# Kernel tuning notes

Hardware: AMD Instinct MI355X
Metric: run time of the kernel (lower is better)

Reference implementation:

```python
import jax, jax.numpy as jnp
import numpy as np

B, LQ, LK, C = 16, 1024, 1024, 512
WH = int(LQ ** 0.5)  # 32


def setup_inputs() -> dict:
    key = jax.random.key(0)
    ks = jax.random.split(key, 6)
    s1 = 1.0 / np.sqrt(LK)
    return {
        "query": jax.random.normal(ks[0], (B, LQ, C), jnp.float32),
        "key": jax.random.normal(ks[1], (B, LK, C), jnp.float32),
        "value": jax.random.normal(ks[2], (B, LK, C), jnp.float32),
        # nn.Linear weights, stored [out_features, in_features] like torch
        "w1": jax.random.normal(ks[3], (LK, LK), jnp.float32) * s1,
        "w2": jax.random.normal(ks[4], (LK, LK), jnp.float32) * s1,
        "w3": jax.random.normal(ks[5], (1, LK), jnp.float32) * s1,
    }


def reference(query, key, value, w1, w2, w3):
    # cosine-similarity matrix (computed under no_grad in the original)
    q = query / 100.0
    k = key / 100.0
    qn = jnp.sqrt(jnp.sum(q * q, axis=-1))[:, :, None]   # [B, LQ, 1]
    kn = jnp.sqrt(jnp.sum(k * k, axis=-1))[:, None, :]   # [B, 1, LK]
    outer = qn * kn                                       # rank-1 outer product [B, LQ, LK]
    upper = jnp.einsum('bqc,bkc->bqk', q, k)              # [B, LQ, LK]
    similar_rev = jax.lax.stop_gradient(upper / (outer + 1e-6))

    # 3-layer MLP gating over the LK axis -> scalar weight per query row
    h = jax.nn.gelu(jnp.einsum('bqk,ok->bqo', similar_rev, w1), approximate=False)
    h = jax.nn.gelu(jnp.einsum('bqk,ok->bqo', h, w2), approximate=False)
    w = jnp.einsum('bqk,ok->bqo', h, w3)[..., 0]          # [B, LQ]

    # weight^T @ similar_rev / wh, then tanh -> per-key scalar gate [B, LK, 1]
    weight = jnp.einsum('bq,bqk->bk', w, similar_rev) / WH
    weight = jnp.tanh(weight)[:, :, None]

    # value modulation + residual
    return value * weight + value
```

## Files before the change

kernel.cpp:

```cpp
#include <hip/hip_runtime.h>
#include <hip/hip_bf16.h>

#define B_  16
#define LQ_ 1024
#define LK_ 1024
#define C_  512

typedef __attribute__((ext_vector_type(4))) float f32x4;
typedef __attribute__((ext_vector_type(8))) short bf16x8;

__device__ __forceinline__ float bf2f(ushort u) {
  union { unsigned int i; float f; } v; v.i = ((unsigned int)u) << 16; return v.f;
}
__device__ __forceinline__ ushort f2bf(float f) {
  union { float f; unsigned int i; } v; v.f = f;
  unsigned int r = v.i + 0x7fffu + ((v.i >> 16) & 1u);
  return (ushort)(r >> 16);
}
__device__ __forceinline__ float gelu_fast(float x) {
  float u = x * (0.7978845608f + 0.0356774081f * x * x);
  u = fminf(fmaxf(u, -9.f), 9.f);
  float e = __expf(2.f * u);
  float t = (e - 1.f) / (e + 1.f);
  return 0.5f * x * (1.f + t);
}

__device__ __forceinline__ void gload_lds16(const ushort* g, ushort* l) {
  __builtin_amdgcn_global_load_lds(
      (const __attribute__((address_space(1))) void*)g,
      (__attribute__((address_space(3))) void*)l, 16, 0, 0);
}

__global__ __launch_bounds__(256) void prep_qk(const float* __restrict__ x,
                                               ushort* __restrict__ xb,
                                               float* __restrict__ norms) {
  int wid = blockIdx.x * 4 + (threadIdx.x >> 6);
  int lane = threadIdx.x & 63;
  const float* xr = x + (long)wid * C_;
  ushort* xo = xb + (long)wid * C_;
  float ss = 0.f;
#pragma unroll
  for (int i0 = 0; i0 < 2; ++i0) {
    int i = lane * 4 + i0 * 256;
    float4 v = *(const float4*)(xr + i);
    ss += v.x * v.x + v.y * v.y + v.z * v.z + v.w * v.w;
    ushort4 o;
    o.x = f2bf(v.x); o.y = f2bf(v.y); o.z = f2bf(v.z); o.w = f2bf(v.w);
    *(ushort4*)(xo + i) = o;
  }
#pragma unroll
  for (int off = 32; off > 0; off >>= 1) ss += __shfl_xor(ss, off);
  if (lane == 0) norms[wid] = sqrtf(ss);
}

__global__ __launch_bounds__(256) void conv_bf16(const float* __restrict__ x,
                                                 ushort* __restrict__ o, int n4) {
  int i = blockIdx.x * 256 + threadIdx.x;
  if (i < n4) {
    float4 v = *(const float4*)(x + (long)i * 4);
    ushort4 u;
    u.x = f2bf(v.x); u.y = f2bf(v.y); u.z = f2bf(v.z); u.w = f2bf(v.w);
    *(ushort4*)(o + (long)i * 4) = u;
  }
}

#define BK 32

template <int EPI>
__device__ __forceinline__ void tile128(
    const ushort* __restrict__ A, const ushort* __restrict__ Bm,
    ushort* __restrict__ Cc, int K, int bm, int bn, int b,
    const float* __restrict__ qn, const float* __restrict__ kn,
    const float* __restrict__ w3v, float* __restrict__ wv,
    ushort* smem) {
  int tid = threadIdx.x;
  int lane = tid & 63, w = tid >> 6;
  int wr = w >> 1, wc = w & 1;
  int l16 = lane & 15, lhi = lane >> 4;

  f32x4 acc[4][4] = {};

  int c0 = tid, c1 = tid + 256;
  int r0 = c0 >> 2, cb0 = (c0 & 3) ^ ((r0 >> 1) & 3);
  int r1 = c1 >> 2, cb1 = (c1 & 3) ^ ((r1 >> 1) & 3);
  int wb0 = (tid & ~63) * 8;
  int wb1 = wb0 + 256 * 8;

  const ushort* Ar0 = A + (long)(bm + r0) * K + cb0 * 8;
  const ushort* Ar1 = A + (long)(bm + r1) * K + cb1 * 8;
  const ushort* Br0 = Bm + (long)(bn + r0) * K + cb0 * 8;
  const ushort* Br1 = Bm + (long)(bn + r1) * K + cb1 * 8;

  const int nt = K / BK;
  gload_lds16(Ar0, smem + wb0);
  gload_lds16(Ar1, smem + wb1);
  gload_lds16(Br0, smem + 8192 + wb0);
  gload_lds16(Br1, smem + 8192 + wb1);
  __syncthreads();

  int cur = 0;
  for (int t = 0; t < nt; ++t) {
    if (t + 1 < nt) {
      int k1 = (t + 1) * BK;
      int nx = (cur ^ 1) * 4096;
      gload_lds16(Ar0 + k1, smem + nx + wb0);
      gload_lds16(Ar1 + k1, smem + nx + wb1);
      gload_lds16(Br0 + k1, smem + 8192 + nx + wb0);
      gload_lds16(Br1 + k1, smem + 8192 + nx + wb1);
    }

    const ushort* Ac = smem + cur * 4096;
    const ushort* Bc = smem + 8192 + cur * 4096;
    bf16x8 af[4], bfr[4];
#pragma unroll
    for (int m = 0; m < 4; ++m) {
      int r = wr * 64 + m * 16 + l16;
      af[m] = *(const bf16x8*)(Ac + r * 32 + ((lhi ^ ((r >> 1) & 3)) * 8));
    }
#pragma unroll
    for (int n = 0; n < 4; ++n) {
      int r = wc * 64 + n * 16 + l16;
      bfr[n] = *(const bf16x8*)(Bc + r * 32 + ((lhi ^ ((r >> 1) & 3)) * 8));
    }
#pragma unroll
    for (int m = 0; m < 4; ++m)
#pragma unroll
      for (int n = 0; n < 4; ++n)
        acc[m][n] = __builtin_amdgcn_mfma_f32_16x16x32_bf16(af[m], bfr[n],
                                                            acc[m][n], 0, 0, 0);
    __syncthreads();
    cur ^= 1;
  }

  if constexpr (EPI == 2) {
    float* wvb = wv + (long)b * LQ_;
    float w3c[4];
#pragma unroll
    for (int n = 0; n < 4; ++n) w3c[n] = w3v[bn + wc * 64 + n * 16 + l16];
#pragma unroll
    for (int m = 0; m < 4; ++m)
#pragma unroll
      for (int rr = 0; rr < 4; ++rr) {
        float s = 0.f;
#pragma unroll
        for (int n = 0; n < 4; ++n)
          s += gelu_fast(acc[m][n][rr]) * w3c[n];
        s += __shfl_xor(s, 1);
        s += __shfl_xor(s, 2);
        s += __shfl_xor(s, 4);
        s += __shfl_xor(s, 8);
        if (l16 == 0)
          atomicAdd(&wvb[bm + wr * 64 + m * 16 + lhi * 4 + rr], s);
      }
  } else {
    const float* qnb = qn + (long)b * LQ_;
    const float* knb = kn + (long)b * LK_;
#pragma unroll
    for (int m = 0; m < 4; ++m) {
      int row0 = bm + wr * 64 + m * 16 + lhi * 4;
#pragma unroll
      for (int n = 0; n < 4; ++n) {
        int col = bn + wc * 64 + n * 16 + l16;
#pragma unroll
        for (int rr = 0; rr < 4; ++rr) {
          float v = acc[m][n][rr];
          int grow = row0 + rr;
          if (EPI == 0) {
            v = v / (qnb[grow] * knb[col] + 1e-2f);
          } else {
            v = gelu_fast(v);
          }
          Cc[(long)grow * 1024 + col] = f2bf(v);
        }
      }
    }
  }
}

template <int EPI>
__device__ __forceinline__ void gemm_pair_body(
    const ushort* __restrict__ A, const ushort* __restrict__ Bm,
    ushort* __restrict__ Cc, int K, long sA, long sB, long sC,
    const float* __restrict__ qn, const float* __restrict__ kn,
    const float* __restrict__ w3v, float* __restrict__ wv) {
  int per = (int)(gridDim.x >> 3);
  int orig = blockIdx.x;
  int id = (orig & 7) * per + (orig >> 3);
  int b = id >> 5;
  int rp = id & 31;
  const int bm = (rp >> 2) * 128, bn0 = (rp & 3) * 256;

  A += (long)b * sA;
  Bm += (long)b * sB;
  if (EPI != 2) Cc += (long)b * sC;

  __shared__ ushort smem[16384];
  tile128<EPI>(A, Bm, Cc, K, bm, bn0, b, qn, kn, w3v, wv, smem);
  tile128<EPI>(A, Bm, Cc, K, bm, bn0 + 128, b, qn, kn, w3v, wv, smem);
}

__global__ __launch_bounds__(256, 2) void gemm_s(
    const ushort* __restrict__ A, const ushort* __restrict__ Bm,
    ushort* __restrict__ Cc, const float* __restrict__ qn,
    const float* __restrict__ kn) {
  gemm_pair_body<0>(A, Bm, Cc, C_, (long)LQ_ * C_, (long)LK_ * C_,
                    (long)LQ_ * LK_, qn, kn, nullptr, nullptr);
}

__global__ __launch_bounds__(256, 2) void gemm_h1(
    const ushort* __restrict__ A, const ushort* __restrict__ Bm,
    ushort* __restrict__ Cc) {
  gemm_pair_body<1>(A, Bm, Cc, LK_, (long)LQ_ * LK_, 0L, (long)LQ_ * LK_,
                    nullptr, nullptr, nullptr, nullptr);
}

__global__ __launch_bounds__(256, 2) void gemm_h2w(
    const ushort* __restrict__ A, const ushort* __restrict__ Bm,
    const float* __restrict__ w3v, float* __restrict__ wv) {
  gemm_pair_body<2>(A, Bm, nullptr, LK_, (long)LQ_ * LK_, 0L, 0L,
                    nullptr, nullptr, w3v, wv);
}

__global__ __launch_bounds__(256) void gate_partial(const ushort* __restrict__ S,
                                                    const float* __restrict__ wv,
                                                    float* __restrict__ wraw) {
  int b = blockIdx.z;
  int k = blockIdx.x * 256 + threadIdx.x;
  int q0 = blockIdx.y * 128;
  const ushort* Sb = S + (long)b * LQ_ * LK_;
  const float* wb = wv + b * LQ_;
  float acc = 0.f;
#pragma unroll 4
  for (int q = q0; q < q0 + 128; ++q) acc += wb[q] * bf2f(Sb[(long)q * LK_ + k]);
  atomicAdd(&wraw[b * LK_ + k], acc);
}

__global__ __launch_bounds__(256) void finalize(const float* __restrict__ value,
                                                const float* __restrict__ wraw,
                                                float* __restrict__ out) {
  long i = (long)blockIdx.x * 256 + threadIdx.x;
  long e = i * 4;
  int row = (int)(e >> 9);
  float g = 1.f + tanhf(wraw[row] * (1.f / 32.f));
  float4 v = ((const float4*)value)[i];
  v.x *= g; v.y *= g; v.z *= g; v.w *= g;
  ((float4*)out)[i] = v;
}

extern "C" void kernel_launch(void* const* d_in, const int* in_sizes, int n_in,
                              void* d_out, int out_size, void* d_ws,
                              size_t ws_size, hipStream_t stream) {
  const float* query = (const float*)d_in[0];
  const float* key   = (const float*)d_in[1];
  const float* value = (const float*)d_in[2];
  const float* w1    = (const float*)d_in[3];
  const float* w2    = (const float*)d_in[4];
  const float* w3    = (const float*)d_in[5];
  float* out = (float*)d_out;

  const size_t QB_BYTES = (size_t)B_ * LQ_ * C_ * 2;
  const size_t S_BYTES  = (size_t)B_ * LQ_ * LK_ * 2;
  const size_t W_BYTES  = (size_t)LK_ * LK_ * 2;
  const size_t OFF_QB = 0;
  const size_t OFF_KB = OFF_QB + QB_BYTES;
  const size_t OFF_S  = OFF_KB + QB_BYTES;
  const size_t OFF_H1 = OFF_S + S_BYTES;
  const size_t OFF_W1 = OFF_H1 + S_BYTES;
  const size_t OFF_W2 = OFF_W1 + W_BYTES;
  const size_t OFF_QN = OFF_W2 + W_BYTES;
  const size_t OFF_KN = OFF_QN + (size_t)B_ * LQ_ * 4;
  const size_t OFF_WV = OFF_KN + (size_t)B_ * LK_ * 4;
  const size_t OFF_WR = OFF_WV + (size_t)B_ * LQ_ * 4;
  const size_t TOTAL  = OFF_WR + (size_t)B_ * LK_ * 4;
  if (ws_size < TOTAL) return;

  char* ws = (char*)d_ws;
  ushort* Qb  = (ushort*)(ws + OFF_QB);
  ushort* Kb  = (ushort*)(ws + OFF_KB);
  ushort* S   = (ushort*)(ws + OFF_S);
  ushort* h1  = (ushort*)(ws + OFF_H1);
  ushort* W1b = (ushort*)(ws + OFF_W1);
  ushort* W2b = (ushort*)(ws + OFF_W2);
  float* qn   = (float*)(ws + OFF_QN);
  float* kn   = (float*)(ws + OFF_KN);
  float* wv   = (float*)(ws + OFF_WV);
  float* wraw = (float*)(ws + OFF_WR);

  prep_qk<<<dim3(B_ * LQ_ / 4), 256, 0, stream>>>(query, Qb, qn);
  prep_qk<<<dim3(B_ * LK_ / 4), 256, 0, stream>>>(key, Kb, kn);
  conv_bf16<<<dim3(LK_ * LK_ / 4 / 256), 256, 0, stream>>>(w1, W1b, LK_ * LK_ / 4);
  conv_bf16<<<dim3(LK_ * LK_ / 4 / 256), 256, 0, stream>>>(w2, W2b, LK_ * LK_ / 4);
  hipMemsetAsync(wraw, 0, (size_t)B_ * LK_ * 4, stream);
  hipMemsetAsync(wv, 0, (size_t)B_ * LQ_ * 4, stream);

  gemm_s<<<dim3(512), 256, 0, stream>>>(Qb, Kb, S, qn, kn);

  gemm_h1<<<dim3(512), 256, 0, stream>>>(S, W1b, h1);

  gemm_h2w<<<dim3(512), 256, 0, stream>>>(h1, W2b, w3, wv);

  gate_partial<<<dim3(LK_ / 256, LQ_ / 128, B_), 256, 0, stream>>>(S, wv, wraw);

  finalize<<<dim3((size_t)B_ * LK_ * C_ / 4 / 256), 256, 0, stream>>>(value, wraw, out);
}
```

Measured before the change: 184.7 us.

## Fuse prep kernels, use one 128x128 tile per GEMM block, vectorize gate

Merges the four conversion/norm launches into one prep kernel that dispatches rows by warp index. Each GEMM block now computes a single 128x128 tile instead of two adjacent tiles, which doubles the grid to 1024 blocks for better CU occupancy and load balance. In exchange, the A-tile reuse across the paired N tiles is lost. The gate reduction now has each thread read four bf16 values with one vector load over 64 query rows, with fewer blocks and more atomics per thread.

```diff
diff --git a/kernel.cpp b/kernel.cpp
--- a/kernel.cpp
+++ b/kernel.cpp
@@ -31,48 +31,66 @@
       (__attribute__((address_space(3))) void*)l, 16, 0, 0);
 }
 
-__global__ __launch_bounds__(256) void prep_qk(const float* __restrict__ x,
-                                               ushort* __restrict__ xb,
-                                               float* __restrict__ norms) {
+__global__ __launch_bounds__(256) void prep_all(
+    const float* __restrict__ q, const float* __restrict__ k,
+    const float* __restrict__ w1, const float* __restrict__ w2,
+    ushort* __restrict__ Qb, ushort* __restrict__ Kb,
+    ushort* __restrict__ W1b, ushort* __restrict__ W2b,
+    float* __restrict__ qn, float* __restrict__ kn) {
   int wid = blockIdx.x * 4 + (threadIdx.x >> 6);
   int lane = threadIdx.x & 63;
-  const float* xr = x + (long)wid * C_;
-  ushort* xo = xb + (long)wid * C_;
+  const float* src;
+  ushort* dst;
+  float* nrm = nullptr;
+  if (wid < 16384) {
+    src = q + (long)wid * C_;  dst = Qb + (long)wid * C_;  nrm = qn + wid;
+  } else if (wid < 32768) {
+    int r = wid - 16384;
+    src = k + (long)r * C_;    dst = Kb + (long)r * C_;    nrm = kn + r;
+  } else if (wid < 34816) {
+    int r = wid - 32768;
+    src = w1 + (long)r * C_;   dst = W1b + (long)r * C_;
+  } else {
+    int r = wid - 34816;
+    src = w2 + (long)r * C_;   dst = W2b + (long)r * C_;
+  }
   float ss = 0.f;
 #pragma unroll
   for (int i0 = 0; i0 < 2; ++i0) {
     int i = lane * 4 + i0 * 256;
-    float4 v = *(const float4*)(xr + i);
+    float4 v = *(const float4*)(src + i);
     ss += v.x * v.x + v.y * v.y + v.z * v.z + v.w * v.w;
     ushort4 o;
     o.x = f2bf(v.x); o.y = f2bf(v.y); o.z = f2bf(v.z); o.w = f2bf(v.w);
-    *(ushort4*)(xo + i) = o;
-  }
-#pragma unroll
-  for (int off = 32; off > 0; off >>= 1) ss += __shfl_xor(ss, off);
-  if (lane == 0) norms[wid] = sqrtf(ss);
-}
-
-__global__ __launch_bounds__(256) void conv_bf16(const float* __restrict__ x,
-                                                 ushort* __restrict__ o, int n4) {
-  int i = blockIdx.x * 256 + threadIdx.x;
-  if (i < n4) {
-    float4 v = *(const float4*)(x + (long)i * 4);
-    ushort4 u;
-    u.x = f2bf(v.x); u.y = f2bf(v.y); u.z = f2bf(v.z); u.w = f2bf(v.w);
-    *(ushort4*)(o + (long)i * 4) = u;
+    *(ushort4*)(dst + i) = o;
+  }
+  if (nrm) {
+#pragma unroll
+    for (int off = 32; off > 0; off >>= 1) ss += __shfl_xor(ss, off);
+    if (lane == 0) *nrm = sqrtf(ss);
   }
 }
 
 #define BK 32
 
 template <int EPI>
-__device__ __forceinline__ void tile128(
+__device__ __forceinline__ void gemm128_body(
     const ushort* __restrict__ A, const ushort* __restrict__ Bm,
-    ushort* __restrict__ Cc, int K, int bm, int bn, int b,
+    ushort* __restrict__ Cc, int K, long sA, long sB, long sC,
     const float* __restrict__ qn, const float* __restrict__ kn,
-    const float* __restrict__ w3v, float* __restrict__ wv,
-    ushort* smem) {
+    const float* __restrict__ w3v, float* __restrict__ wv) {
+  int per = (int)(gridDim.x >> 3);
+  int orig = blockIdx.x;
+  int id = (orig & 7) * per + (orig >> 3);
+  int b = id >> 6;
+  int rtile = id & 63;
+  const int bm = (rtile >> 3) * 128, bn = (rtile & 7) * 128;
+
+  A += (long)b * sA;
+  Bm += (long)b * sB;
+
+  __shared__ ushort smem[16384];
+
   int tid = threadIdx.x;
   int lane = tid & 63, w = tid >> 6;
   int wr = w >> 1, wc = w & 1;
@@ -153,6 +171,7 @@
           atomicAdd(&wvb[bm + wr * 64 + m * 16 + lhi * 4 + rr], s);
       }
   } else {
+    Cc += (long)b * sC;
     const float* qnb = qn + (long)b * LQ_;
     const float* knb = kn + (long)b * LK_;
 #pragma unroll
@@ -177,62 +196,51 @@
   }
 }
 
-template <int EPI>
-__device__ __forceinline__ void gemm_pair_body(
-    const ushort* __restrict__ A, const ushort* __restrict__ Bm,
-    ushort* __restrict__ Cc, int K, long sA, long sB, long sC,
-    const float* __restrict__ qn, const float* __restrict__ kn,
-    const float* __restrict__ w3v, float* __restrict__ wv) {
-  int per = (int)(gridDim.x >> 3);
-  int orig = blockIdx.x;
-  int id = (orig & 7) * per + (orig >> 3);
-  int b = id >> 5;
-  int rp = id & 31;
-  const int bm = (rp >> 2) * 128, bn0 = (rp & 3) * 256;
-
-  A += (long)b * sA;
-  Bm += (long)b * sB;
-  if (EPI != 2) Cc += (long)b * sC;
-
-  __shared__ ushort smem[16384];
-  tile128<EPI>(A, Bm, Cc, K, bm, bn0, b, qn, kn, w3v, wv, smem);
-  tile128<EPI>(A, Bm, Cc, K, bm, bn0 + 128, b, qn, kn, w3v, wv, smem);
-}
-
 __global__ __launch_bounds__(256, 2) void gemm_s(
     const ushort* __restrict__ A, const ushort* __restrict__ Bm,
     ushort* __restrict__ Cc, const float* __restrict__ qn,
     const float* __restrict__ kn) {
-  gemm_pair_body<0>(A, Bm, Cc, C_, (long)LQ_ * C_, (long)LK_ * C_,
-                    (long)LQ_ * LK_, qn, kn, nullptr, nullptr);
+  gemm128_body<0>(A, Bm, Cc, C_, (long)LQ_ * C_, (long)LK_ * C_,
+                  (long)LQ_ * LK_, qn, kn, nullptr, nullptr);
 }
 
 __global__ __launch_bounds__(256, 2) void gemm_h1(
     const ushort* __restrict__ A, const ushort* __restrict__ Bm,
     ushort* __restrict__ Cc) {
-  gemm_pair_body<1>(A, Bm, Cc, LK_, (long)LQ_ * LK_, 0L, (long)LQ_ * LK_,
-                    nullptr, nullptr, nullptr, nullptr);
+  gemm128_body<1>(A, Bm, Cc, LK_, (long)LQ_ * LK_, 0L, (long)LQ_ * LK_,
+                  nullptr, nullptr, nullptr, nullptr);
 }
 
 __global__ __launch_bounds__(256, 2) void gemm_h2w(
     const ushort* __restrict__ A, const ushort* __restrict__ Bm,
     const float* __restrict__ w3v, float* __restrict__ wv) {
-  gemm_pair_body<2>(A, Bm, nullptr, LK_, (long)LQ_ * LK_, 0L, 0L,
-                    nullptr, nullptr, w3v, wv);
+  gemm128_body<2>(A, Bm, nullptr, LK_, (long)LQ_ * LK_, 0L, 0L,
+                  nullptr, nullptr, w3v, wv);
 }
 
 __global__ __launch_bounds__(256) void gate_partial(const ushort* __restrict__ S,
                                                     const float* __restrict__ wv,
                                                     float* __restrict__ wraw) {
   int b = blockIdx.z;
-  int k = blockIdx.x * 256 + threadIdx.x;
-  int q0 = blockIdx.y * 128;
-  const ushort* Sb = S + (long)b * LQ_ * LK_;
-  const float* wb = wv + b * LQ_;
-  float acc = 0.f;
+  int q0 = blockIdx.y * 64;
+  int k4 = threadIdx.x * 4;
+  const ushort* p = S + (long)b * LQ_ * LK_ + (long)q0 * LK_ + k4;
+  const float* wb = wv + b * LQ_ + q0;
+  float a0 = 0.f, a1 = 0.f, a2 = 0.f, a3 = 0.f;
 #pragma unroll 4
-  for (int q = q0; q < q0 + 128; ++q) acc += wb[q] * bf2f(Sb[(long)q * LK_ + k]);
-  atomicAdd(&wraw[b * LK_ + k], acc);
+  for (int q = 0; q < 64; ++q) {
+    float wq = wb[q];
+    ushort4 s4 = *(const ushort4*)(p + (long)q * LK_);
+    a0 += wq * bf2f(s4.x);
+    a1 += wq * bf2f(s4.y);
+    a2 += wq * bf2f(s4.z);
+    a3 += wq * bf2f(s4.w);
+  }
+  float* wr = wraw + b * LK_ + k4;
+  atomicAdd(wr + 0, a0);
+  atomicAdd(wr + 1, a1);
+  atomicAdd(wr + 2, a2);
+  atomicAdd(wr + 3, a3);
 }
 
 __global__ __launch_bounds__(256) void finalize(const float* __restrict__ value,
@@ -286,20 +294,18 @@
   float* wv   = (float*)(ws + OFF_WV);
   float* wraw = (float*)(ws + OFF_WR);
 
-  prep_qk<<<dim3(B_ * LQ_ / 4), 256, 0, stream>>>(query, Qb, qn);
-  prep_qk<<<dim3(B_ * LK_ / 4), 256, 0, stream>>>(key, Kb, kn);
-  conv_bf16<<<dim3(LK_ * LK_ / 4 / 256), 256, 0, stream>>>(w1, W1b, LK_ * LK_ / 4);
-  conv_bf16<<<dim3(LK_ * LK_ / 4 / 256), 256, 0, stream>>>(w2, W2b, LK_ * LK_ / 4);
+  prep_all<<<dim3(9216), 256, 0, stream>>>(query, key, w1, w2, Qb, Kb, W1b,
+                                           W2b, qn, kn);
   hipMemsetAsync(wraw, 0, (size_t)B_ * LK_ * 4, stream);
   hipMemsetAsync(wv, 0, (size_t)B_ * LQ_ * 4, stream);
 
-  gemm_s<<<dim3(512), 256, 0, stream>>>(Qb, Kb, S, qn, kn);
-
-  gemm_h1<<<dim3(512), 256, 0, stream>>>(S, W1b, h1);
-
-  gemm_h2w<<<dim3(512), 256, 0, stream>>>(h1, W2b, w3, wv);
-
-  gate_partial<<<dim3(LK_ / 256, LQ_ / 128, B_), 256, 0, stream>>>(S, wv, wraw);
+  gemm_s<<<dim3(1024), 256, 0, stream>>>(Qb, Kb, S, qn, kn);
+
+  gemm_h1<<<dim3(1024), 256, 0, stream>>>(S, W1b, h1);
+
+  gemm_h2w<<<dim3(1024), 256, 0, stream>>>(h1, W2b, w3, wv);
+
+  gate_partial<<<dim3(1, 16, B_), 256, 0, stream>>>(S, wv, wraw);
 
   finalize<<<dim3((size_t)B_ * LK_ * C_ / 4 / 256), 256, 0, stream>>>(value, wraw, out);
 }
```

Result: faster. 171.3 us (-7.2%).
